# Kernel tuning notes

Hardware: AMD Instinct MI355X
Metric: run time of the kernel (lower is better)

The kernel has to match this reference:

```python
import jax, jax.numpy as jnp
import numpy as np

# Model config (matches init_kwargs)
B, J, D_IN, D_MODEL, NUM_HEADS, NUM_LAYERS = 1024, 24, 64, 512, 8, 6
A = J + 1  # joints + cls token
LN_EPS = 1e-5


def setup_inputs() -> dict:
    key = jax.random.key(0)
    ks = jax.random.split(key, 14)
    s = 0.02  # weight init scale
    return {
        "x": jax.random.normal(ks[0], (B, J, D_IN), dtype=jnp.float32),
        # per-joint input embeddings: Linear(d_in, d_model) x J
        "We": jax.random.normal(ks[1], (J, D_IN, D_MODEL), dtype=jnp.float32) * s,
        "be": jnp.zeros((J, D_MODEL), dtype=jnp.float32),
        "cls_token": jax.random.normal(ks[2], (D_MODEL,), dtype=jnp.float32),
        # per-layer shared key/value projections
        "Wk": jax.random.normal(ks[3], (NUM_LAYERS, D_MODEL, D_MODEL), dtype=jnp.float32) * s,
        "bk": jnp.zeros((NUM_LAYERS, D_MODEL), dtype=jnp.float32),
        "Wv": jax.random.normal(ks[4], (NUM_LAYERS, D_MODEL, D_MODEL), dtype=jnp.float32) * s,
        "bv": jnp.zeros((NUM_LAYERS, D_MODEL), dtype=jnp.float32),
        # per-layer, PER-JOINT query projections (ModuleList of A linears)
        "Wq": jax.random.normal(ks[5], (NUM_LAYERS, A, D_MODEL, D_MODEL), dtype=jnp.float32) * s,
        "bq": jnp.zeros((NUM_LAYERS, A, D_MODEL), dtype=jnp.float32),
        "Wo": jax.random.normal(ks[6], (NUM_LAYERS, D_MODEL, D_MODEL), dtype=jnp.float32) * s,
        "bo": jnp.zeros((NUM_LAYERS, D_MODEL), dtype=jnp.float32),
        "ln_g": jnp.ones((NUM_LAYERS, D_MODEL), dtype=jnp.float32),
        "ln_b": jnp.zeros((NUM_LAYERS, D_MODEL), dtype=jnp.float32),
    }


def _layernorm(y, g, b):
    m = jnp.mean(y, axis=-1, keepdims=True)
    v = jnp.var(y, axis=-1, keepdims=True)  # ddof=0 matches torch LayerNorm
    return (y - m) * jax.lax.rsqrt(v + LN_EPS) * g + b


def reference(x, We, be, cls_token, Wk, bk, Wv, bv, Wq, bq, Wo, bo, ln_g, ln_b):
    b = x.shape[0]
    depth = D_MODEL // NUM_HEADS
    # per-joint input embedding -> (B, J, D)
    tok = jnp.einsum("bjd,jde->bje", x, We) + be
    cls = jnp.broadcast_to(cls_token[None, None, :], (b, 1, D_MODEL))
    h = jnp.concatenate([cls, tok], axis=1)  # (B, A, D); the seq dim of 1 is dropped

    def split(t):  # (B, A, D) -> (B, H, A, depth)
        return t.reshape(b, A, NUM_HEADS, depth).transpose(0, 2, 1, 3)

    for l in range(NUM_LAYERS):
        k = h @ Wk[l] + bk[l]                                  # (B, A, D)
        v = h @ Wv[l] + bv[l]                                  # (B, A, D)
        q = jnp.einsum("bad,ade->bae", h, Wq[l]) + bq[l]        # per-joint query
        qh, kh, vh = split(q), split(k), split(v)
        scores = jnp.einsum("bhqd,bhkd->bhqk", qh, kh) / jnp.sqrt(jnp.float32(depth))
        w = jax.nn.softmax(scores, axis=-1)                    # (B, H, A, A)
        o = jnp.einsum("bhqk,bhkd->bhqd", w, vh)
        o = o.transpose(0, 2, 1, 3).reshape(b, A, D_MODEL)
        o = o @ Wo[l] + bo[l]
        h = _layernorm(h + o, ln_g[l], ln_b[l])
    return h  # (B, A, D) == inputs[:, 0, :, :] in the torch code
```

## Files before the change

kernel.cpp:

```cpp
#include <hip/hip_runtime.h>

typedef unsigned short u16;
typedef unsigned int u32;
typedef short bf16x8 __attribute__((ext_vector_type(8)));
typedef float f32x4 __attribute__((ext_vector_type(4)));

#define AS1 __attribute__((address_space(1)))
#define AS3 __attribute__((address_space(3)))

__device__ __forceinline__ u16 f2b(float f) {
  u32 u = __float_as_uint(f);
  u += 0x7fffu + ((u >> 16) & 1u);
  return (u16)(u >> 16);
}
__device__ __forceinline__ float b2f(u16 s) {
  return __uint_as_float(((u32)s) << 16);
}

__device__ __forceinline__ void gload16(const u16* g, u16* l) {
  __builtin_amdgcn_global_load_lds((const AS1 void*)g, (AS3 void*)l, 16, 0, 0);
}

__global__ __launch_bounds__(256) void prep_kernel(const float* __restrict__ x,
                                                   const float* __restrict__ cls,
                                                   u16* __restrict__ xb,
                                                   u16* __restrict__ hb) {
  if (blockIdx.x < 1536) {
    int i = blockIdx.x * 256 + threadIdx.x;
    float4 v = ((const float4*)x)[i];
    ushort4 u;
    u.x = f2b(v.x); u.y = f2b(v.y); u.z = f2b(v.z); u.w = f2b(v.w);
    ((ushort4*)xb)[i] = u;
  } else {
    int i = (blockIdx.x - 1536) * 256 + threadIdx.x;
    int b = i >> 7;
    int e = (i & 127) << 2;
    float4 v = *(const float4*)(cls + e);
    long off = (long)b * (25 * 512) + e;
    ushort4 u;
    u.x = f2b(v.x); u.y = f2b(v.y); u.z = f2b(v.z); u.w = f2b(v.w);
    *(ushort4*)(hb + off) = u;
  }
}

__global__ __launch_bounds__(256) void convT_kernel(const float* __restrict__ src,
                                                    u16* __restrict__ dst,
                                                    int K, int N,
                                                    long src_gstride, long dst_gstride) {
  __shared__ float t[64][65];
  const int k0 = blockIdx.x * 64, n0 = blockIdx.y * 64;
  const float* s = src + (long)blockIdx.z * src_gstride;
  u16* d = dst + (long)blockIdx.z * dst_gstride;
  for (int i = threadIdx.x; i < 4096; i += 256) {
    int r = i >> 6, c = i & 63;
    t[r][c] = s[(long)(k0 + r) * N + n0 + c];
  }
  __syncthreads();
  for (int i = threadIdx.x; i < 4096; i += 256) {
    int r = i >> 6, c = i & 63;
    d[(long)(n0 + r) * K + k0 + c] = f2b(t[c][r]);
  }
}

__global__ __launch_bounds__(256) void convT4_kernel(
    const float* __restrict__ wq, const float* __restrict__ wk,
    const float* __restrict__ wv, const float* __restrict__ wo,
    u16* __restrict__ dq, u16* __restrict__ dk,
    u16* __restrict__ dv, u16* __restrict__ dwo) {
  __shared__ float t[64][65];
  const int z = blockIdx.z;
  const float* src;
  u16* dst;
  if (z < 25)      { src = wq + (long)z * 262144; dst = dq + (long)z * 262144; }
  else if (z == 25){ src = wk; dst = dk; }
  else if (z == 26){ src = wv; dst = dv; }
  else             { src = wo; dst = dwo; }
  const int k0 = blockIdx.x * 64, n0 = blockIdx.y * 64;
  for (int i = threadIdx.x; i < 4096; i += 256) {
    int r = i >> 6, c = i & 63;
    t[r][c] = src[(long)(k0 + r) * 512 + n0 + c];
  }
  __syncthreads();
  for (int i = threadIdx.x; i < 4096; i += 256) {
    int r = i >> 6, c = i & 63;
    dst[(long)(n0 + r) * 512 + k0 + c] = f2b(t[c][r]);
  }
}

__device__ __forceinline__ void gemm_core(u16* lds,
    const u16* Ag, long a_stride, const u16* Wg, const float* biasg,
    u16* Cg, long c_stride, int K, int m0, int n0) {
  u16* As0 = lds;
  u16* Bs0 = lds + 8192;
  u16* As1 = lds + 16384;
  u16* Bs1 = lds + 24576;

  const int tid = threadIdx.x;
  const int lane = tid & 63;
  const int wave = tid >> 6;
  const int wr = wave >> 1, wc = wave & 1;

  const int schunk = lane & 7;
  const u16* ga[4];
  const u16* gb[4];
  int lo[4];
#pragma unroll
  for (int i = 0; i < 4; ++i) {
    const int r = wave * 32 + i * 8 + (lane >> 3);
    const int csw = (schunk ^ (r & 7)) << 3;
    ga[i] = Ag + (long)(m0 + r) * a_stride + csw;
    gb[i] = Wg + (long)(n0 + r) * K + csw;
    lo[i] = (wave * 32 + i * 8) * 64;
  }

  f32x4 acc[4][4];
#pragma unroll
  for (int m = 0; m < 4; ++m)
#pragma unroll
    for (int n = 0; n < 4; ++n) {
      acc[m][n][0] = 0.f; acc[m][n][1] = 0.f;
      acc[m][n][2] = 0.f; acc[m][n][3] = 0.f;
    }

  auto STAGE = [&](int k0, u16* A, u16* B) {
#pragma unroll
    for (int i = 0; i < 4; ++i) {
      gload16(ga[i] + k0, A + lo[i]);
      gload16(gb[i] + k0, B + lo[i]);
    }
  };
  auto COMPUTE = [&](const u16* A, const u16* B) {
#pragma unroll
    for (int kk = 0; kk < 64; kk += 32) {
      const int kb = kk + ((lane >> 4) << 3);
      bf16x8 af[4], bfr[4];
#pragma unroll
      for (int m = 0; m < 4; ++m) {
        const int R = (wr << 6) + (m << 4) + (lane & 15);
        af[m] = *(const bf16x8*)&A[((R << 6) + kb) ^ ((R & 7) << 3)];
      }
#pragma unroll
      for (int n = 0; n < 4; ++n) {
        const int Cc = (wc << 6) + (n << 4) + (lane & 15);
        bfr[n] = *(const bf16x8*)&B[((Cc << 6) + kb) ^ ((Cc & 7) << 3)];
      }
#pragma unroll
      for (int m = 0; m < 4; ++m)
#pragma unroll
        for (int n = 0; n < 4; ++n)
          acc[m][n] = __builtin_amdgcn_mfma_f32_16x16x32_bf16(af[m], bfr[n],
                                                              acc[m][n], 0, 0, 0);
    }
  };

  const int nt = K >> 6;
  STAGE(0, As0, Bs0);
  __syncthreads();
  for (int t = 0; t < nt; ++t) {
    u16* cA = (t & 1) ? As1 : As0;
    u16* cB = (t & 1) ? Bs1 : Bs0;
    if (t + 1 < nt) {
      u16* nA = (t & 1) ? As0 : As1;
      u16* nB = (t & 1) ? Bs0 : Bs1;
      STAGE((t + 1) << 6, nA, nB);
    }
    COMPUTE(cA, cB);
    if (t + 1 < nt) __syncthreads();
  }

  const int lcol = lane & 15;
  const int lrow = (lane >> 4) << 2;
#pragma unroll
  for (int n = 0; n < 4; ++n) {
    const int col = n0 + (wc << 6) + (n << 4) + lcol;
    const float bv = biasg[col];
#pragma unroll
    for (int m = 0; m < 4; ++m) {
      const int row = m0 + (wr << 6) + (m << 4) + lrow;
#pragma unroll
      for (int j = 0; j < 4; ++j) {
        const float val = acc[m][n][j] + bv;
        Cg[(long)(row + j) * c_stride + col] = f2b(val);
      }
    }
  }
}

__global__ __launch_bounds__(256) void gemm_plain(
    const u16* __restrict__ Abase, long a_stride, long a_goff,
    const u16* __restrict__ Wbase, long w_gstride,
    const float* __restrict__ biasbase, long bias_gstride,
    u16* __restrict__ Cb, long c_stride, long c_goff, int K) {
  __shared__ u16 lds[4 * 8192];
  const int gx = gridDim.x, gy = gridDim.y;
  int lin = blockIdx.x + gx * (blockIdx.y + gy * blockIdx.z);
  const int total = gx * gy * gridDim.z;
  const int chunk = total >> 3;
  lin = (lin & 7) * chunk + (lin >> 3);
  const int g = lin / (gx * gy);
  const int rem = lin % (gx * gy);
  const int mt = rem % gx;
  const int nt = rem / gx;
  gemm_core(lds,
            Abase + (long)g * a_goff, a_stride,
            Wbase + (long)g * w_gstride,
            biasbase + (long)g * bias_gstride,
            Cb + (long)g * c_goff, c_stride, K,
            mt * 128, nt * 128);
}

__global__ __launch_bounds__(256) void gemm_qkv(
    const u16* __restrict__ hb,
    const u16* __restrict__ wqT, const u16* __restrict__ wkT, const u16* __restrict__ wvT,
    const float* __restrict__ bq, const float* __restrict__ bk, const float* __restrict__ bv,
    u16* __restrict__ qb, u16* __restrict__ kb, u16* __restrict__ vb) {
  __shared__ u16 lds[4 * 8192];
  const int bid = (blockIdx.x & 7) * 300 + (blockIdx.x >> 3);
  const u16* Ag; long a_str; const u16* Wg; const float* bg; u16* Cg; long c_str;
  int mt, nt;
  if (bid < 800) {
    const int g = bid >> 5, rem = bid & 31;
    mt = rem >> 2; nt = rem & 3;
    Ag = hb + (long)g * 512; a_str = 12800;
    Wg = wqT + (long)g * 262144; bg = bq + (long)g * 512;
    Cg = qb + (long)g * 512; c_str = 12800;
  } else if (bid < 1600) {
    const int rem = bid - 800;
    mt = rem >> 2; nt = rem & 3;
    Ag = hb; a_str = 512; Wg = wkT; bg = bk; Cg = kb; c_str = 512;
  } else {
    const int rem = bid - 1600;
    mt = rem >> 2; nt = rem & 3;
    Ag = hb; a_str = 512; Wg = wvT; bg = bv; Cg = vb; c_str = 512;
  }
  gemm_core(lds, Ag, a_str, Wg, bg, Cg, c_str, 512, mt * 128, nt * 128);
}

__global__ __launch_bounds__(256) void attn_kernel(const u16* __restrict__ q,
                                                   u16* __restrict__ kio,
                                                   const u16* __restrict__ v) {
  __shared__ float ks_[25 * 256];
  __shared__ float vs_[25 * 256];
  const int tid = threadIdx.x;
  const int b = blockIdx.x >> 1;
  const int h0 = blockIdx.x & 1;
  const long base = (long)b * 25 * 512;

  for (int i = tid; i < 800; i += 256) {
    const int j = i >> 5, c = i & 31;
    const long goff = base + (long)j * 512 + h0 * 256 + c * 8;
    uint4 kt = *(const uint4*)(kio + goff);
    uint4 vt = *(const uint4*)(v + goff);
    const u32 ka[4] = {kt.x, kt.y, kt.z, kt.w};
    const u32 va[4] = {vt.x, vt.y, vt.z, vt.w};
    float4 k0f = {b2f((u16)ka[0]), b2f((u16)(ka[0] >> 16)),
                  b2f((u16)ka[1]), b2f((u16)(ka[1] >> 16))};
    float4 k1f = {b2f((u16)ka[2]), b2f((u16)(ka[2] >> 16)),
                  b2f((u16)ka[3]), b2f((u16)(ka[3] >> 16))};
    float4 v0f = {b2f((u16)va[0]), b2f((u16)(va[0] >> 16)),
                  b2f((u16)va[1]), b2f((u16)(va[1] >> 16))};
    float4 v1f = {b2f((u16)va[2]), b2f((u16)(va[2] >> 16)),
                  b2f((u16)va[3]), b2f((u16)(va[3] >> 16))};
    const int off = j * 256 + c * 8;
    *(float4*)&ks_[off]     = k0f;
    *(float4*)&ks_[off + 4] = k1f;
    *(float4*)&vs_[off]     = v0f;
    *(float4*)&vs_[off + 4] = v1f;
  }
  __syncthreads();

  const int w = tid >> 6;
  const int lane = tid & 63;
  const int qi = lane >> 1;
  const int half = lane & 1;
  if (qi < 25) {
    const int h = h0 * 4 + w;
    const int dslice = w * 64 + half * 32;

    const u16* qrow = q + base + (long)qi * 512 + h * 64 + half * 32;
    float buf[32];
#pragma unroll
    for (int c = 0; c < 4; ++c) {
      uint4 t = *(const uint4*)(qrow + c * 8);
      const u32 tt[4] = {t.x, t.y, t.z, t.w};
#pragma unroll
      for (int e = 0; e < 4; ++e) {
        buf[c * 8 + 2 * e]     = b2f((u16)tt[e]);
        buf[c * 8 + 2 * e + 1] = b2f((u16)(tt[e] >> 16));
      }
    }

    float sc[25];
    float mx = -1e30f;
#pragma unroll
    for (int j = 0; j < 25; ++j) {
      const float4* kr = (const float4*)&ks_[j * 256 + dslice];
      float s0 = 0.f, s1 = 0.f;
#pragma unroll
      for (int c4 = 0; c4 < 8; ++c4) {
        float4 kv = kr[c4];
        s0 += buf[4 * c4 + 0] * kv.x + buf[4 * c4 + 1] * kv.y;
        s1 += buf[4 * c4 + 2] * kv.z + buf[4 * c4 + 3] * kv.w;
      }
      float s = s0 + s1;
      s += __shfl_xor(s, 1);
      s *= 0.125f;
      sc[j] = s;
      mx = fmaxf(mx, s);
    }
    float sum = 0.f;
#pragma unroll
    for (int j = 0; j < 25; ++j) {
      sc[j] = __expf(sc[j] - mx);
      sum += sc[j];
    }
    const float inv = 1.f / sum;

#pragma unroll
    for (int d = 0; d < 32; ++d) buf[d] = 0.f;
#pragma unroll
    for (int j = 0; j < 25; ++j) {
      const float wj = sc[j];
      const float4* vr = (const float4*)&vs_[j * 256 + dslice];
#pragma unroll
      for (int c4 = 0; c4 < 8; ++c4) {
        float4 vv = vr[c4];
        buf[4 * c4 + 0] += wj * vv.x;
        buf[4 * c4 + 1] += wj * vv.y;
        buf[4 * c4 + 2] += wj * vv.z;
        buf[4 * c4 + 3] += wj * vv.w;
      }
    }

    u16* orow = kio + base + (long)qi * 512 + h * 64 + half * 32;
#pragma unroll
    for (int c = 0; c < 4; ++c) {
      uint4 t;
      u32 tt[4];
#pragma unroll
      for (int e = 0; e < 4; ++e)
        tt[e] = (u32)f2b(buf[c * 8 + 2 * e] * inv) |
                ((u32)f2b(buf[c * 8 + 2 * e + 1] * inv) << 16);
      t.x = tt[0]; t.y = tt[1]; t.z = tt[2]; t.w = tt[3];
      *(uint4*)(orow + c * 8) = t;
    }
  }
}

__global__ __launch_bounds__(256) void ln_kernel(u16* hb,
                                                 const u16* __restrict__ o,
                                                 const float* __restrict__ g,
                                                 const float* __restrict__ bta,
                                                 float* fout) {
  const int lane = threadIdx.x & 63;
  const int wave = threadIdx.x >> 6;
  const long row = (long)blockIdx.x * 4 + wave;
  u16* hr = hb + row * 512;
  const u16* orow = o + row * 512;
  const int base = lane << 3;
  uint4 hv4 = *(const uint4*)(hr + base);
  uint4 ov = *(const uint4*)(orow + base);
  const u32 ha[4] = {hv4.x, hv4.y, hv4.z, hv4.w};
  const u32 oa[4] = {ov.x, ov.y, ov.z, ov.w};
  float y[8];
#pragma unroll
  for (int e = 0; e < 4; ++e) {
    y[2 * e]     = b2f((u16)ha[e])         + b2f((u16)oa[e]);
    y[2 * e + 1] = b2f((u16)(ha[e] >> 16)) + b2f((u16)(oa[e] >> 16));
  }
  float s = 0.f, ss = 0.f;
#pragma unroll
  for (int i = 0; i < 8; ++i) { s += y[i]; ss += y[i] * y[i]; }
#pragma unroll
  for (int off = 32; off > 0; off >>= 1) {
    s += __shfl_down(s, off);
    ss += __shfl_down(ss, off);
  }
  s = __shfl(s, 0);
  ss = __shfl(ss, 0);
  const float mean = s * (1.f / 512.f);
  const float var = ss * (1.f / 512.f) - mean * mean;
  const float rinv = rsqrtf(var + 1e-5f);
  float4 g0 = *(const float4*)(g + base);
  float4 g1 = *(const float4*)(g + base + 4);
  float4 b0 = *(const float4*)(bta + base);
  float4 b1 = *(const float4*)(bta + base + 4);
  float r[8];
  r[0] = (y[0] - mean) * rinv * g0.x + b0.x;
  r[1] = (y[1] - mean) * rinv * g0.y + b0.y;
  r[2] = (y[2] - mean) * rinv * g0.z + b0.z;
  r[3] = (y[3] - mean) * rinv * g0.w + b0.w;
  r[4] = (y[4] - mean) * rinv * g1.x + b1.x;
  r[5] = (y[5] - mean) * rinv * g1.y + b1.y;
  r[6] = (y[6] - mean) * rinv * g1.z + b1.z;
  r[7] = (y[7] - mean) * rinv * g1.w + b1.w;
  uint4 hv;
  hv.x = (u32)f2b(r[0]) | ((u32)f2b(r[1]) << 16);
  hv.y = (u32)f2b(r[2]) | ((u32)f2b(r[3]) << 16);
  hv.z = (u32)f2b(r[4]) | ((u32)f2b(r[5]) << 16);
  hv.w = (u32)f2b(r[6]) | ((u32)f2b(r[7]) << 16);
  *(uint4*)(hr + base) = hv;
  if (fout) {
    float* fr = fout + row * 512 + base;
    float4 w0 = {r[0], r[1], r[2], r[3]};
    float4 w1 = {r[4], r[5], r[6], r[7]};
    *(float4*)(fr) = w0;
    *(float4*)(fr + 4) = w1;
  }
}

extern "C" void kernel_launch(void* const* d_in, const int* in_sizes, int n_in,
                              void* d_out, int out_size, void* d_ws, size_t ws_size,
                              hipStream_t stream) {
  const float* x   = (const float*)d_in[0];
  const float* We  = (const float*)d_in[1];
  const float* be  = (const float*)d_in[2];
  const float* cls = (const float*)d_in[3];
  const float* Wk  = (const float*)d_in[4];
  const float* bk  = (const float*)d_in[5];
  const float* Wv  = (const float*)d_in[6];
  const float* bv  = (const float*)d_in[7];
  const float* Wq  = (const float*)d_in[8];
  const float* bq  = (const float*)d_in[9];
  const float* Wo  = (const float*)d_in[10];
  const float* bo  = (const float*)d_in[11];
  const float* lng = (const float*)d_in[12];
  const float* lnb = (const float*)d_in[13];
  float* out = (float*)d_out;

  char* ws = (char*)d_ws;
  u16* hb = (u16*)ws;
  u16* kb = (u16*)(ws + 26214400);
  u16* vb = (u16*)(ws + 52428800);
  u16* qb = (u16*)(ws + 78643200);
  u16* xb = kb;

  u16* scr = (u16*)d_out;
  u16* weT = scr;
  u16* wqT = scr;
  u16* wkT = scr + 6553600;
  u16* wvT = scr + 6815744;
  u16* woT = scr + 7077888;

  prep_kernel<<<2048, 256, 0, stream>>>(x, cls, xb, hb);
  convT_kernel<<<dim3(1, 8, 24), 256, 0, stream>>>(We, weT, 64, 512, 32768, 32768);
  gemm_plain<<<dim3(8, 4, 24), 256, 0, stream>>>(
      xb, 1536, 64, weT, 32768, be, 512, hb + 512, 12800, 512, 64);

  for (int l = 0; l < 6; ++l) {
    convT4_kernel<<<dim3(8, 8, 28), 256, 0, stream>>>(
        Wq + (long)l * 6553600, Wk + (long)l * 262144,
        Wv + (long)l * 262144, Wo + (long)l * 262144,
        wqT, wkT, wvT, woT);
    gemm_qkv<<<2400, 256, 0, stream>>>(
        hb, wqT, wkT, wvT,
        bq + (long)l * 12800, bk + (long)l * 512, bv + (long)l * 512,
        qb, kb, vb);
    attn_kernel<<<2048, 256, 0, stream>>>(qb, kb, vb);
    gemm_plain<<<dim3(200, 4, 1), 256, 0, stream>>>(
        kb, 512, 0, woT, 0, bo + (long)l * 512, 0, qb, 512, 0, 512);
    ln_kernel<<<6400, 256, 0, stream>>>(hb, qb, lng + l * 512, lnb + l * 512,
                                        (l == 5) ? out : nullptr);
  }
}
```

Measured before the change: 1.013 ms.

## Overlap next-layer weight conversion with QKV GEMM and relax GEMM barriers

Each layer's weight transpose/bf16 conversion, which used to be its own kernel launch, now runs as extra blocks appended to the previous layer's QKV GEMM launch. The converted weights are double-buffered in the output scratch, so converting layer l+1 does not clash with the reads of layer l. The GEMM main loop also swaps __syncthreads for explicit s_barrier and partial vmcnt waits, so the next tile's loads can stay in flight during compute. The aim is fewer launches and overlap of memory-bound conversion with compute, at the cost of a larger scratch footprint in the output buffer and hand-written wait counts that must match the number of loads issued.

```diff
diff --git a/kernel.cpp b/kernel.cpp
--- a/kernel.cpp
+++ b/kernel.cpp
@@ -43,23 +43,29 @@
   }
 }
 
+__device__ __forceinline__ void conv_tile(const float* __restrict__ src,
+                                          u16* __restrict__ dst,
+                                          int K, int N, int k0, int n0,
+                                          void* smem) {
+  float (*t)[65] = (float(*)[65])smem;
+  for (int i = threadIdx.x; i < 4096; i += 256) {
+    int r = i >> 6, c = i & 63;
+    t[r][c] = src[(long)(k0 + r) * N + n0 + c];
+  }
+  __syncthreads();
+  for (int i = threadIdx.x; i < 4096; i += 256) {
+    int r = i >> 6, c = i & 63;
+    dst[(long)(n0 + r) * K + k0 + c] = f2b(t[c][r]);
+  }
+}
+
 __global__ __launch_bounds__(256) void convT_kernel(const float* __restrict__ src,
                                                     u16* __restrict__ dst,
                                                     int K, int N,
                                                     long src_gstride, long dst_gstride) {
   __shared__ float t[64][65];
-  const int k0 = blockIdx.x * 64, n0 = blockIdx.y * 64;
-  const float* s = src + (long)blockIdx.z * src_gstride;
-  u16* d = dst + (long)blockIdx.z * dst_gstride;
-  for (int i = threadIdx.x; i < 4096; i += 256) {
-    int r = i >> 6, c = i & 63;
-    t[r][c] = s[(long)(k0 + r) * N + n0 + c];
-  }
-  __syncthreads();
-  for (int i = threadIdx.x; i < 4096; i += 256) {
-    int r = i >> 6, c = i & 63;
-    d[(long)(n0 + r) * K + k0 + c] = f2b(t[c][r]);
-  }
+  conv_tile(src + (long)blockIdx.z * src_gstride, dst + (long)blockIdx.z * dst_gstride,
+            K, N, blockIdx.x * 64, blockIdx.y * 64, t);
 }
 
 __global__ __launch_bounds__(256) void convT4_kernel(
@@ -75,16 +81,7 @@
   else if (z == 25){ src = wk; dst = dk; }
   else if (z == 26){ src = wv; dst = dv; }
   else             { src = wo; dst = dwo; }
-  const int k0 = blockIdx.x * 64, n0 = blockIdx.y * 64;
-  for (int i = threadIdx.x; i < 4096; i += 256) {
-    int r = i >> 6, c = i & 63;
-    t[r][c] = src[(long)(k0 + r) * 512 + n0 + c];
-  }
-  __syncthreads();
-  for (int i = threadIdx.x; i < 4096; i += 256) {
-    int r = i >> 6, c = i & 63;
-    dst[(long)(n0 + r) * 512 + k0 + c] = f2b(t[c][r]);
-  }
+  conv_tile(src, dst, 512, 512, blockIdx.x * 64, blockIdx.y * 64, t);
 }
 
 __device__ __forceinline__ void gemm_core(u16* lds,
@@ -155,17 +152,22 @@
 
   const int nt = K >> 6;
   STAGE(0, As0, Bs0);
-  __syncthreads();
   for (int t = 0; t < nt; ++t) {
     u16* cA = (t & 1) ? As1 : As0;
     u16* cB = (t & 1) ? Bs1 : Bs0;
+    __builtin_amdgcn_s_barrier();
+    __builtin_amdgcn_sched_barrier(0);
     if (t + 1 < nt) {
       u16* nA = (t & 1) ? As0 : As1;
       u16* nB = (t & 1) ? Bs0 : Bs1;
       STAGE((t + 1) << 6, nA, nB);
-    }
+      asm volatile("s_waitcnt vmcnt(8)" ::: "memory");
+    } else {
+      asm volatile("s_waitcnt vmcnt(0)" ::: "memory");
+    }
+    __builtin_amdgcn_s_barrier();
+    __builtin_amdgcn_sched_barrier(0);
     COMPUTE(cA, cB);
-    if (t + 1 < nt) __syncthreads();
   }
 
   const int lcol = lane & 15;
@@ -191,7 +193,7 @@
     const u16* __restrict__ Wbase, long w_gstride,
     const float* __restrict__ biasbase, long bias_gstride,
     u16* __restrict__ Cb, long c_stride, long c_goff, int K) {
-  __shared__ u16 lds[4 * 8192];
+  __shared__ u16 lds[32768];
   const int gx = gridDim.x, gy = gridDim.y;
   int lin = blockIdx.x + gx * (blockIdx.y + gy * blockIdx.z);
   const int total = gx * gy * gridDim.z;
@@ -213,8 +215,26 @@
     const u16* __restrict__ hb,
     const u16* __restrict__ wqT, const u16* __restrict__ wkT, const u16* __restrict__ wvT,
     const float* __restrict__ bq, const float* __restrict__ bk, const float* __restrict__ bv,
-    u16* __restrict__ qb, u16* __restrict__ kb, u16* __restrict__ vb) {
-  __shared__ u16 lds[4 * 8192];
+    u16* __restrict__ qb, u16* __restrict__ kb, u16* __restrict__ vb,
+    const float* __restrict__ nwq, const float* __restrict__ nwk,
+    const float* __restrict__ nwv, const float* __restrict__ nwo,
+    u16* __restrict__ ndq, u16* __restrict__ ndk,
+    u16* __restrict__ ndv, u16* __restrict__ ndwo) {
+  __shared__ u16 lds[32768];
+  if (blockIdx.x >= 2400) {
+    const int idx = blockIdx.x - 2400;
+    const int z = idx >> 6;
+    const int rem = idx & 63;
+    const int k0 = (rem & 7) * 64, n0 = (rem >> 3) * 64;
+    const float* src;
+    u16* dst;
+    if (z < 25)      { src = nwq + (long)z * 262144; dst = ndq + (long)z * 262144; }
+    else if (z == 25){ src = nwk; dst = ndk; }
+    else if (z == 26){ src = nwv; dst = ndv; }
+    else             { src = nwo; dst = ndwo; }
+    conv_tile(src, dst, 512, 512, k0, n0, lds);
+    return;
+  }
   const int bid = (blockIdx.x & 7) * 300 + (blockIdx.x >> 3);
   const u16* Ag; long a_str; const u16* Wg; const float* bg; u16* Cg; long c_str;
   int mt, nt;
@@ -436,29 +456,32 @@
   u16* xb = kb;
 
   u16* scr = (u16*)d_out;
-  u16* weT = scr;
-  u16* wqT = scr;
-  u16* wkT = scr + 6553600;
-  u16* wvT = scr + 6815744;
-  u16* woT = scr + 7077888;
+  const long SCR = 7340032;
+  u16* weT = scr + 2 * SCR;
 
   prep_kernel<<<2048, 256, 0, stream>>>(x, cls, xb, hb);
   convT_kernel<<<dim3(1, 8, 24), 256, 0, stream>>>(We, weT, 64, 512, 32768, 32768);
+  convT4_kernel<<<dim3(8, 8, 28), 256, 0, stream>>>(
+      Wq, Wk, Wv, Wo, scr, scr + 6553600, scr + 6815744, scr + 7077888);
   gemm_plain<<<dim3(8, 4, 24), 256, 0, stream>>>(
       xb, 1536, 64, weT, 32768, be, 512, hb + 512, 12800, 512, 64);
 
   for (int l = 0; l < 6; ++l) {
-    convT4_kernel<<<dim3(8, 8, 28), 256, 0, stream>>>(
-        Wq + (long)l * 6553600, Wk + (long)l * 262144,
-        Wv + (long)l * 262144, Wo + (long)l * 262144,
-        wqT, wkT, wvT, woT);
-    gemm_qkv<<<2400, 256, 0, stream>>>(
-        hb, wqT, wkT, wvT,
+    u16* cw = scr + (l & 1) * SCR;
+    u16* nw = scr + ((l + 1) & 1) * SCR;
+    const bool conv = (l < 5);
+    gemm_qkv<<<conv ? 4192 : 2400, 256, 0, stream>>>(
+        hb, cw, cw + 6553600, cw + 6815744,
         bq + (long)l * 12800, bk + (long)l * 512, bv + (long)l * 512,
-        qb, kb, vb);
+        qb, kb, vb,
+        conv ? Wq + (long)(l + 1) * 6553600 : Wq,
+        conv ? Wk + (long)(l + 1) * 262144 : Wk,
+        conv ? Wv + (long)(l + 1) * 262144 : Wv,
+        conv ? Wo + (long)(l + 1) * 262144 : Wo,
+        nw, nw + 6553600, nw + 6815744, nw + 7077888);
     attn_kernel<<<2048, 256, 0, stream>>>(qb, kb, vb);
     gemm_plain<<<dim3(200, 4, 1), 256, 0, stream>>>(
-        kb, 512, 0, woT, 0, bo + (long)l * 512, 0, qb, 512, 0, 512);
+        kb, 512, 0, cw + 7077888, 0, bo + (long)l * 512, 0, qb, 512, 0, 512);
     ln_kernel<<<6400, 256, 0, stream>>>(hb, qb, lng + l * 512, lnb + l * 512,
                                         (l == 5) ? out : nullptr);
   }
```

New measurement: 1.073 ms. 1.06x slower.
